# Kernel tuning notes

Hardware: AMD Instinct MI355X
Metric: run time of the kernel (lower is better)

Reference implementation:

```python
import jax, jax.numpy as jnp
import numpy as np


def _relative_position_index(S):
    # Faithful to the torch buffer construction, computed once with numpy (static).
    coords = np.stack(np.meshgrid(np.arange(S), np.arange(S), indexing='ij'))  # (2,S,S)
    coords = coords.reshape(2, -1)                                             # (2,N)
    rel = coords[:, :, None] - coords[:, None, :]                              # (2,N,N)
    rel = rel.transpose(1, 2, 0).astype(np.int64)                              # (N,N,2)
    rel[:, :, 0] += S - 1
    rel[:, :, 1] += S - 1
    rel[:, :, 0] *= 2 * S - 1
    idx = rel.sum(-1)
    idx = idx[::-1, ::-1].copy()  # flipud(fliplr(...))
    return idx                    # (N,N) int64 in [0, (2S-1)^2)


def setup_inputs() -> dict:
    key = jax.random.key(0)
    ks = jax.random.split(key, 6)
    B, S, C, NH = 8, 32, 512, 16
    x = jax.random.normal(ks[0], (B, S, S, C), dtype=jnp.float32)
    qkv_w = jax.random.normal(ks[1], (3 * C, C), dtype=jnp.float32) * 0.02
    qkv_b = jax.random.normal(ks[2], (3 * C,), dtype=jnp.float32) * 0.02
    rpb = jax.random.normal(ks[3], (NH, 2 * S - 1, 2 * S - 1), dtype=jnp.float32) * 0.02
    proj_w = jax.random.normal(ks[4], (C, C), dtype=jnp.float32) * 0.02
    proj_b = jax.random.normal(ks[5], (C,), dtype=jnp.float32) * 0.02
    return {"x": x, "qkv_w": qkv_w, "qkv_b": qkv_b, "rpb": rpb,
            "proj_w": proj_w, "proj_b": proj_b}


def reference(x, qkv_w, qkv_b, rpb, proj_w, proj_b):
    B, H, W, C = x.shape
    N = H * W
    num_heads = rpb.shape[0]
    head_dim = C // num_heads
    scale = head_dim ** (-0.5)
    S = H

    idx = _relative_position_index(S)  # static numpy (N,N)

    qkv = x.reshape(B, N, C) @ qkv_w.T + qkv_b            # (B,N,3C)
    qkv = qkv.reshape(B, N, 3, num_heads, head_dim)
    qkv = jnp.transpose(qkv, (2, 0, 3, 1, 4))             # (3,B,h,N,d)
    q, k, v = qkv[0], qkv[1], qkv[2]

    attn = jnp.einsum('bhnd,bhmd->bhnm', q * scale, k)    # (B,h,N,N)
    # gather relative position bias: (h,(2S-1)^2)[:, idx] -> (h,N,N)
    bias = rpb.reshape(num_heads, -1)[:, idx]
    attn = jax.nn.softmax(attn + bias[None], axis=-1)

    out = jnp.einsum('bhnm,bhmd->bhnd', attn, v)          # (B,h,N,d)
    out = jnp.transpose(out, (0, 2, 1, 3)).reshape(B, H, W, C)
    return out @ proj_w.T + proj_b
```

## Files before the change

kernel.cpp:

```cpp
#include <hip/hip_runtime.h>

typedef __bf16 bf16x8 __attribute__((ext_vector_type(8)));
typedef float f32x4 __attribute__((ext_vector_type(4)));
typedef unsigned short u16;
typedef unsigned int u32;

__device__ __forceinline__ float bf2f(u16 v) {
    union { unsigned u; float f; } x; x.u = ((unsigned)v) << 16; return x.f;
}
__device__ __forceinline__ u16 f2bf(float f) {
    union { float f; unsigned u; } x; x.f = f;
    unsigned r = x.u + 0x7fffu + ((x.u >> 16) & 1u);
    return (u16)(r >> 16);
}

__device__ __forceinline__ bool probe_is_f32(const void* xp) {
    const unsigned* p = (const unsigned*)xp;
    int hits = 0;
#pragma unroll
    for (int i = 0; i < 32; i++) {
        const unsigned e = (p[i] >> 7) & 0xffu;
        hits += (e >= 0x90u) ? 1 : 0;
    }
    return hits > 3;
}

__device__ __forceinline__ float ld1(const void* p, size_t i, bool isf32) {
    return isf32 ? ((const float*)p)[i] : bf2f(((const u16*)p)[i]);
}

__device__ __forceinline__ void gl2lds16(const void* g, void* l) {
    __builtin_amdgcn_global_load_lds(
        (const __attribute__((address_space(1))) u32*)g,
        (__attribute__((address_space(3))) u32*)l, 16, 0, 0);
}

__global__ __launch_bounds__(256)
void convert_inputs(const void* __restrict__ x, const void* __restrict__ qw,
                    const void* __restrict__ qb, const void* __restrict__ pw,
                    const void* __restrict__ pb, const void* __restrict__ rp,
                    u16* __restrict__ xbf, u16* __restrict__ qwbf,
                    u16* __restrict__ qbbf, u16* __restrict__ pwbf,
                    u16* __restrict__ pbbf, float* __restrict__ rpl2e)
{
    const bool isf32 = probe_is_f32(x);
    const int gid = blockIdx.x * 256 + threadIdx.x;
    const int gsz = gridDim.x * 256;

    struct Seg { const void* s; u16* d; int n; };
    const Seg segs[5] = {{x, xbf, 4194304}, {qw, qwbf, 786432}, {pw, pwbf, 262144},
                         {qb, qbbf, 1536}, {pb, pbbf, 512}};
    for (int t = 0; t < 5; t++) {
        const int n4 = segs[t].n >> 2;
        if (isf32) {
            const f32x4* s = (const f32x4*)segs[t].s;
            for (int i = gid; i < n4; i += gsz) {
                f32x4 v = s[i];
                ushort4 o;
                o.x = f2bf(v[0]); o.y = f2bf(v[1]); o.z = f2bf(v[2]); o.w = f2bf(v[3]);
                *(ushort4*)(segs[t].d + i * 4) = o;
            }
        } else {
            const ushort4* s = (const ushort4*)segs[t].s;
            for (int i = gid; i < n4; i += gsz) *(ushort4*)(segs[t].d + i * 4) = s[i];
        }
    }
    for (int i = gid; i < 63504; i += gsz)
        rpl2e[i] = ld1(rp, i, isf32) * 1.4426950408889634f;
}

template<int MODE, int BM>
__global__ __launch_bounds__(256, MODE == 1 ? 3 : 4)
void gemm_bt(const u16* __restrict__ A, const u16* __restrict__ W,
             const u16* __restrict__ bias, void* __restrict__ out,
             u16* __restrict__ q_out, u16* __restrict__ k_out, u16* __restrict__ v_out,
             const void* __restrict__ probe, int Nout, int K)
{
    __shared__ __align__(16) u16 As[2][BM * 32];
    __shared__ __align__(16) u16 Ws[2][128 * 32];
    constexpr int RW = BM / 32;

    const int tid  = threadIdx.x;
    const int lane = tid & 63;
    const int wave = tid >> 6;
    const int quad = lane >> 4;
    const int l16  = lane & 15;
    const int m0 = blockIdx.y * BM;
    const int n0 = blockIdx.x * 128;
    const int wm = (wave >> 1) * (BM / 2);
    const int wn = (wave & 1) * 64;

    f32x4 acc[RW][4] = {};

    for (int k0 = 0; k0 < K; k0 += 64) {
        __syncthreads();
        for (int u = 0; u < 2; u++) {
            {
                const u16* g = A + (size_t)(m0 + wave * 16 + (lane >> 2)) * K
                                 + k0 + u * 32 + (lane & 3) * 8;
                u16* l = As[u] + wave * 16 * 32;
                for (int p = 0; p < BM / 64; p++) gl2lds16(g + (size_t)p * 64 * K, l + p * 64 * 32);
            }
            {
                const u16* g = W + (size_t)(n0 + wave * 16 + (lane >> 2)) * K
                                 + k0 + u * 32 + (lane & 3) * 8;
                u16* l = Ws[u] + wave * 16 * 32;
                for (int p = 0; p < 2; p++) gl2lds16(g + (size_t)p * 64 * K, l + p * 64 * 32);
            }
        }
        __syncthreads();

        for (int u = 0; u < 2; u++) {
            bf16x8 af[RW], wf[4];
            for (int i = 0; i < RW; i++)
                af[i] = *(const bf16x8*)(As[u] + (wm + i * 16 + l16) * 32 + quad * 8);
            for (int j = 0; j < 4; j++)
                wf[j] = *(const bf16x8*)(Ws[u] + (wn + j * 16 + l16) * 32 + quad * 8);
            for (int i = 0; i < RW; i++)
                for (int j = 0; j < 4; j++)
                    acc[i][j] = __builtin_amdgcn_mfma_f32_16x16x32_bf16(af[i], wf[j], acc[i][j], 0, 0, 0);
        }
    }

    if (MODE == 0) {
        const bool isf32 = probe_is_f32(probe);
        for (int j = 0; j < 4; j++) {
            const int col = n0 + wn + j * 16 + l16;
            const float bv = bf2f(bias[col]);
            for (int i = 0; i < RW; i++) {
                const int rbase = m0 + wm + i * 16 + quad * 4;
                for (int r = 0; r < 4; r++) {
                    const float val = acc[i][j][r] + bv;
                    if (isf32) ((float*)out)[(size_t)(rbase + r) * Nout + col] = val;
                    else       ((u16*)out)[(size_t)(rbase + r) * Nout + col]  = f2bf(val);
                }
            }
        }
    } else {
        const int which = m0 >> 9;
        float bv[RW][4];
        for (int i = 0; i < RW; i++) {
            const int row4 = m0 + wm + i * 16 + quad * 4;
            for (int r = 0; r < 4; r++) bv[i][r] = bf2f(bias[row4 + r]);
        }
        for (int j = 0; j < 4; j++) {
            const int tok = n0 + wn + j * 16 + l16;
            const int bi = tok >> 10, t = tok & 1023;
            for (int i = 0; i < RW; i++) {
                const int row4 = m0 + wm + i * 16 + quad * 4;
                const int h = (row4 >> 5) & 15;
                const int c = row4 & 31;
                if (which == 2) {
                    for (int r = 0; r < 4; r++)
                        v_out[((size_t)(bi * 16 + h) * 32 + c + r) * 1024 + t] =
                            f2bf(acc[i][j][r] + bv[i][r]);
                } else {
                    u16* dst = which ? k_out : q_out;
                    ushort4 pk;
                    pk.x = f2bf(acc[i][j][0] + bv[i][0]);
                    pk.y = f2bf(acc[i][j][1] + bv[i][1]);
                    pk.z = f2bf(acc[i][j][2] + bv[i][2]);
                    pk.w = f2bf(acc[i][j][3] + bv[i][3]);
                    *(ushort4*)(dst + ((size_t)(bi * 16 + h) * 1024 + t) * 32 + c) = pk;
                }
            }
        }
    }
}

__global__ __launch_bounds__(256, 4)
void attn(const u16* __restrict__ q, const u16* __restrict__ k,
          const u16* __restrict__ vt, const float* __restrict__ rpl2e,
          u16* __restrict__ o)
{
    __shared__ __align__(16) u16 Ks[2][64 * 40];
    __shared__ __align__(16) u16 Vt[2][32 * 72];
    __shared__ __align__(16) u16 Ps[4][16 * 72];
    __shared__ float biasS[35 * 63];

    const int tid  = threadIdx.x;
    const int lane = tid & 63;
    const int wave = tid >> 6;
    const int quad = lane >> 4;
    const int l16  = lane & 15;

    const int h  = blockIdx.x;
    const int qt = blockIdx.y;
    const int b  = blockIdx.z;
    const int n0 = qt * 128;
    const size_t base = ((size_t)(b * 16 + h)) * 32768;

    {
        const int row0 = 28 - 4 * qt;
        for (int idx = tid; idx < 2205; idx += 256)
            biasS[idx] = rpl2e[(size_t)h * 3969 + (size_t)(row0 + idx / 63) * 63 + idx % 63];
    }
    uint4 kreg = *(const uint4*)(k + base + (size_t)(tid >> 2) * 32 + (tid & 3) * 8);
    uint4 vreg = *(const uint4*)(vt + base + (size_t)(tid >> 3) * 1024 + (tid & 7) * 8);
    *(uint4*)(Ks[0] + (tid >> 2) * 40 + (tid & 3) * 8) = kreg;
    *(uint4*)(Vt[0] + (tid >> 3) * 72 + (tid & 7) * 8) = vreg;

    bf16x8 qf[2];
    for (int g = 0; g < 2; g++) {
        union { uint4 u; bf16x8 f; } cv;
        cv.u = *(const uint4*)(q + base + (size_t)(n0 + g * 64 + wave * 16 + l16) * 32 + quad * 8);
        qf[g] = cv.f;
    }
    __syncthreads();

    bf16x8 ones;
    for (int i = 0; i < 8; i++) ones[i] = (__bf16)1.0f;

    f32x4 o_acc[2][3] = {};
    const int bn = (wave & 1) * 16 + l16;
    const float SC = 0.25503485724582146f;
    u16* pw = Ps[wave];

    for (int kt = 0; kt < 16; kt++) {
        const int cur = kt & 1;
        if (kt < 15) {
            const int mn = (kt + 1) * 64;
            kreg = *(const uint4*)(k + base + (size_t)(mn + (tid >> 2)) * 32 + (tid & 3) * 8);
            vreg = *(const uint4*)(vt + base + (size_t)(tid >> 3) * 1024 + mn + (tid & 7) * 8);
        }

        bf16x8 kf[4];
        for (int j = 0; j < 4; j++)
            kf[j] = *(const bf16x8*)(Ks[cur] + (j * 16 + l16) * 40 + quad * 8);
        bf16x8 vf[2][2];
        for (int kc = 0; kc < 2; kc++)
            for (int ct = 0; ct < 2; ct++)
                vf[kc][ct] = *(const bf16x8*)(Vt[cur] + (ct * 16 + l16) * 72 + kc * 32 + quad * 8);

        for (int g = 0; g < 2; g++) {
            f32x4 s4[4];
            const f32x4 zero = {};
            for (int j = 0; j < 4; j++)
                s4[j] = __builtin_amdgcn_mfma_f32_16x16x32_bf16(kf[j], qf[g], zero, 0, 0, 0);

            const int rbase = 2 * kt - (wave >> 1) - 2 * g + 3;
            for (int j = 0; j < 4; j++) {
                const float* brow = biasS + (rbase + (j >> 1)) * 63
                                   + ((j & 1) * 16 + quad * 4) - bn + 31;
                ushort4 pk;
                u16* pks = (u16*)&pk;
                for (int r = 0; r < 4; r++) {
                    const float pv = __builtin_amdgcn_exp2f(s4[j][r] * SC + brow[r]);
                    union { __bf16 b; u16 u; } cv; cv.b = (__bf16)pv;
                    pks[r] = cv.u;
                }
                *(ushort4*)(pw + l16 * 72 + j * 16 + quad * 4) = pk;
            }

            for (int kc = 0; kc < 2; kc++) {
                const bf16x8 pa = *(const bf16x8*)(pw + l16 * 72 + kc * 32 + quad * 8);
                for (int ct = 0; ct < 2; ct++)
                    o_acc[g][ct] = __builtin_amdgcn_mfma_f32_16x16x32_bf16(pa, vf[kc][ct], o_acc[g][ct], 0, 0, 0);
                o_acc[g][2] = __builtin_amdgcn_mfma_f32_16x16x32_bf16(pa, ones, o_acc[g][2], 0, 0, 0);
            }
        }

        if (kt < 15) {
            *(uint4*)(Ks[cur ^ 1] + (tid >> 2) * 40 + (tid & 3) * 8) = kreg;
            *(uint4*)(Vt[cur ^ 1] + (tid >> 3) * 72 + (tid & 7) * 8) = vreg;
        }
        __syncthreads();
    }

    for (int g = 0; g < 2; g++)
        for (int r = 0; r < 4; r++) {
            const float inv = __builtin_amdgcn_rcpf(o_acc[g][2][r]);
            const int n = n0 + g * 64 + wave * 16 + quad * 4 + r;
            u16* orow = o + ((size_t)b * 1024 + n) * 512 + h * 32;
            orow[l16]      = f2bf(o_acc[g][0][r] * inv);
            orow[16 + l16] = f2bf(o_acc[g][1][r] * inv);
        }
}

extern "C" void kernel_launch(void* const* d_in, const int* in_sizes, int n_in,
                              void* d_out, int out_size, void* d_ws, size_t ws_size,
                              hipStream_t stream) {
    const void* x      = d_in[0];
    const void* qkv_w  = d_in[1];
    const void* qkv_b  = d_in[2];
    const void* rpb    = d_in[3];
    const void* proj_w = d_in[4];
    const void* proj_b = d_in[5];

    u16* ws    = (u16*)d_ws;
    u16* kb    = ws;
    u16* vb    = ws + 4194304;
    u16* xbf   = ws + 8388608;
    u16* ao    = xbf;
    u16* qwbf  = ws + 12582912;
    u16* pwbf  = ws + 13369344;
    u16* qbbf  = ws + 13631488;
    u16* pbbf  = ws + 13633024;
    float* rpl2e = (float*)(ws + 13633536);
    u16* qb    = (u16*)d_out;

    convert_inputs<<<1024, 256, 0, stream>>>(x, qkv_w, qkv_b, proj_w, proj_b, rpb,
                                             xbf, qwbf, qbbf, pwbf, pbbf, rpl2e);

    dim3 g1(8192 / 128, 1536 / 128);
    gemm_bt<1, 128><<<g1, 256, 0, stream>>>(qwbf, xbf, qbbf, nullptr, qb, kb, vb, x, 8192, 512);

    dim3 g2(16, 8, 8);
    attn<<<g2, 256, 0, stream>>>(qb, kb, vb, rpl2e, ao);

    dim3 g3(512 / 128, 8192 / 64);
    gemm_bt<0, 64><<<g3, 256, 0, stream>>>(ao, pwbf, pbbf, d_out, nullptr, nullptr, nullptr, x, 512, 512);
}
```

Before: 151.2 us.

## Load K/V fragments directly from global memory and drop LDS staging and barriers

Removes the double-buffered shared-memory staging of K and V tiles, along with the per-iteration __syncthreads. Each wave now loads its MFMA operand fragments straight from global memory, relying on L1/L2 caching since all four waves read the same tiles. It also raises wave priority around the MFMA groups with s_setprio. The trade-off is less LDS use and no block barriers, at the cost of redundant global loads per wave and exposed load latency, since there is no explicit prefetch of the next tile.

```diff
diff --git a/kernel.cpp b/kernel.cpp
--- a/kernel.cpp
+++ b/kernel.cpp
@@ -173,8 +173,6 @@
           const u16* __restrict__ vt, const float* __restrict__ rpl2e,
           u16* __restrict__ o)
 {
-    __shared__ __align__(16) u16 Ks[2][64 * 40];
-    __shared__ __align__(16) u16 Vt[2][32 * 72];
     __shared__ __align__(16) u16 Ps[4][16 * 72];
     __shared__ float biasS[35 * 63];
 
@@ -195,10 +193,6 @@
         for (int idx = tid; idx < 2205; idx += 256)
             biasS[idx] = rpl2e[(size_t)h * 3969 + (size_t)(row0 + idx / 63) * 63 + idx % 63];
     }
-    uint4 kreg = *(const uint4*)(k + base + (size_t)(tid >> 2) * 32 + (tid & 3) * 8);
-    uint4 vreg = *(const uint4*)(vt + base + (size_t)(tid >> 3) * 1024 + (tid & 7) * 8);
-    *(uint4*)(Ks[0] + (tid >> 2) * 40 + (tid & 3) * 8) = kreg;
-    *(uint4*)(Vt[0] + (tid >> 3) * 72 + (tid & 7) * 8) = vreg;
 
     bf16x8 qf[2];
     for (int g = 0; g < 2; g++) {
@@ -217,26 +211,29 @@
     u16* pw = Ps[wave];
 
     for (int kt = 0; kt < 16; kt++) {
-        const int cur = kt & 1;
-        if (kt < 15) {
-            const int mn = (kt + 1) * 64;
-            kreg = *(const uint4*)(k + base + (size_t)(mn + (tid >> 2)) * 32 + (tid & 3) * 8);
-            vreg = *(const uint4*)(vt + base + (size_t)(tid >> 3) * 1024 + mn + (tid & 7) * 8);
-        }
-
-        bf16x8 kf[4];
-        for (int j = 0; j < 4; j++)
-            kf[j] = *(const bf16x8*)(Ks[cur] + (j * 16 + l16) * 40 + quad * 8);
-        bf16x8 vf[2][2];
+        const int mn = kt * 64;
+
+        bf16x8 kf[4], vf[2][2];
+        for (int j = 0; j < 4; j++) {
+            union { uint4 u; bf16x8 f; } cv;
+            cv.u = *(const uint4*)(k + base + (size_t)(mn + j * 16 + l16) * 32 + quad * 8);
+            kf[j] = cv.f;
+        }
         for (int kc = 0; kc < 2; kc++)
-            for (int ct = 0; ct < 2; ct++)
-                vf[kc][ct] = *(const bf16x8*)(Vt[cur] + (ct * 16 + l16) * 72 + kc * 32 + quad * 8);
+            for (int ct = 0; ct < 2; ct++) {
+                union { uint4 u; bf16x8 f; } cv;
+                cv.u = *(const uint4*)(vt + base + (size_t)(ct * 16 + l16) * 1024
+                                       + mn + kc * 32 + quad * 8);
+                vf[kc][ct] = cv.f;
+            }
 
         for (int g = 0; g < 2; g++) {
             f32x4 s4[4];
             const f32x4 zero = {};
+            __builtin_amdgcn_s_setprio(1);
             for (int j = 0; j < 4; j++)
                 s4[j] = __builtin_amdgcn_mfma_f32_16x16x32_bf16(kf[j], qf[g], zero, 0, 0, 0);
+            __builtin_amdgcn_s_setprio(0);
 
             const int rbase = 2 * kt - (wave >> 1) - 2 * g + 3;
             for (int j = 0; j < 4; j++) {
@@ -252,19 +249,15 @@
                 *(ushort4*)(pw + l16 * 72 + j * 16 + quad * 4) = pk;
             }
 
+            __builtin_amdgcn_s_setprio(1);
             for (int kc = 0; kc < 2; kc++) {
                 const bf16x8 pa = *(const bf16x8*)(pw + l16 * 72 + kc * 32 + quad * 8);
                 for (int ct = 0; ct < 2; ct++)
                     o_acc[g][ct] = __builtin_amdgcn_mfma_f32_16x16x32_bf16(pa, vf[kc][ct], o_acc[g][ct], 0, 0, 0);
                 o_acc[g][2] = __builtin_amdgcn_mfma_f32_16x16x32_bf16(pa, ones, o_acc[g][2], 0, 0, 0);
             }
-        }
-
-        if (kt < 15) {
-            *(uint4*)(Ks[cur ^ 1] + (tid >> 2) * 40 + (tid & 3) * 8) = kreg;
-            *(uint4*)(Vt[cur ^ 1] + (tid >> 3) * 72 + (tid & 7) * 8) = vreg;
-        }
-        __syncthreads();
+            __builtin_amdgcn_s_setprio(0);
+        }
     }
 
     for (int g = 0; g < 2; g++)
```

New measurement: 163.5 us. +8.1%, slower.
